# Kernel tuning notes

Hardware: AMD Instinct MI355X
Metric: run time of the kernel (lower is better)

## Reference

```python
import math
import jax, jax.numpy as jnp
import numpy as np

B, T, D = 2048, 50, 256
NEG = -100000.0

def setup_inputs() -> dict:
    key = jax.random.key(0)
    ks = jax.random.split(key, 9)
    return {
        "x": jax.random.normal(ks[0], (B, T, D), dtype=jnp.float32),
        "mask": jax.random.randint(ks[1], (B, T, 1), 0, 2, dtype=jnp.int32),
        "time_decay": jax.random.uniform(ks[2], (B, T, 1), dtype=jnp.float32),
        "Wq": jax.random.normal(ks[3], (D, D), dtype=jnp.float32) * (1.0 / math.sqrt(D)),
        "bq": jax.random.normal(ks[4], (D,), dtype=jnp.float32) * 0.01,
        "Wk": jax.random.normal(ks[5], (D, D), dtype=jnp.float32) * (1.0 / math.sqrt(D)),
        "bk": jax.random.normal(ks[6], (D,), dtype=jnp.float32) * 0.01,
        "Wv": jax.random.normal(ks[7], (D, D), dtype=jnp.float32) * (1.0 / math.sqrt(D)),
        "bv": jax.random.normal(ks[8], (D,), dtype=jnp.float32) * 0.01,
    }

def reference(x, mask, time_decay, Wq, bq, Wk, bk, Wv, bv):
    # PositionalEncoding.forward: elementwise multiply by time-decay (broadcast over d_model)
    x = x * time_decay  # [B,T,D]
    q = jnp.einsum('btd,ed->bte', x, Wq) + bq
    k = jnp.einsum('btd,ed->bte', x, Wk) + bk
    v = jnp.einsum('btd,ed->bte', x, Wv) + bv
    # unusual Q/K-side masking (masked_fill before the matmul)
    keep = mask != 0  # [B,T,1]
    q = jnp.where(keep, q, NEG)
    k = jnp.where(keep, k, NEG)
    score = jnp.einsum('btd,bsd->bts', q, k) / math.sqrt(D)  # [B,T,T]
    score = jax.nn.softmax(score, axis=-1)
    # dropout is identity in eval mode
    out = jnp.einsum('bts,bsd->btd', score, v)  # [B,T,D]
    return out[:, -1, :]  # [B,D]
```

## Files before the change

kernel.cpp:

```cpp
#include <hip/hip_runtime.h>


namespace {
constexpr int kB = 2048;
constexpr int kT = 50;
constexpr int kD = 256;
constexpr int kThr = 256;
constexpr double kNeg = -100000.0;
constexpr int oM2 = 0;
constexpr int oWvp = 65536;
constexpr int oV0 = 131072;
constexpr int oC = 131328;
constexpr int oW1 = 131584;
constexpr int oW2 = 131840;
constexpr int oDbl = 132096;
constexpr int oSq = 132608;
constexpr int oQbk = 136704;
constexpr int oU = 140800;
}

__global__ __launch_bounds__(kThr) void precomp(
    const float* __restrict__ Wq, const float* __restrict__ bq,
    const float* __restrict__ Wk, const float* __restrict__ bk,
    const float* __restrict__ Wv, float* __restrict__ ws) {
  const int t = threadIdx.x;
  const int wave = t >> 6;
  const int lane = t & 63;
  const int blk = blockIdx.x;
  __shared__ float coefL[kD];
  __shared__ double red[3][4];

  if (blk < 256) {
    const int a = blk;
    coefL[t] = Wq[(size_t)t * kD + a];
    __syncthreads();
    const float* kcol = Wk + t;
    float pre[8];
#pragma unroll
    for (int k = 0; k < 8; ++k) pre[k] = kcol[(size_t)k * kD];
    float acc = 0.f;
    for (int j0 = 0; j0 < kD; j0 += 8) {
      float cur[8];
#pragma unroll
      for (int k = 0; k < 8; ++k) cur[k] = pre[k];
      const int nx = (j0 + 8 < kD) ? (j0 + 8) : 0;
#pragma unroll
      for (int k = 0; k < 8; ++k) pre[k] = kcol[(size_t)(nx + k) * kD];
#pragma unroll
      for (int k = 0; k < 8; ++k) acc += coefL[j0 + k] * cur[k];
    }
    ws[oM2 + (a >> 2) * 1024 + 4 * t + (a & 3)] = acc;
  } else if (blk < 258) {
    const float* W = (blk == 256) ? Wk : Wq;
    const float* coef = (blk == 256) ? bq : bk;
    coefL[t] = coef[t];
    __syncthreads();
    const float* col = W + t;
    float pre[8];
#pragma unroll
    for (int k = 0; k < 8; ++k) pre[k] = col[(size_t)k * kD];
    double a0 = 0.0, a1 = 0.0;
    for (int j0 = 0; j0 < kD; j0 += 8) {
      float cur[8];
#pragma unroll
      for (int k = 0; k < 8; ++k) cur[k] = pre[k];
      const int nx = (j0 + 8 < kD) ? (j0 + 8) : 0;
#pragma unroll
      for (int k = 0; k < 8; ++k) pre[k] = col[(size_t)(nx + k) * kD];
#pragma unroll
      for (int k = 0; k < 8; ++k) {
        const double w = (double)cur[k];
        a0 += (double)coefL[j0 + k] * w;
        a1 += w;
      }
    }
    if (blk == 256) {
      ws[oV0 + t] = (float)a0;
      ws[oC + t] = (float)a1;
    } else {
      ws[oW1 + t] = (float)a0;
      ws[oW2 + t] = (float)a1;
      double p0 = (double)bk[t];
      double p1 = (double)bq[t] * (double)bk[t];
      double p2 = (double)bq[t];
#pragma unroll
      for (int off = 32; off; off >>= 1) {
        p0 += __shfl_xor(p0, off);
        p1 += __shfl_xor(p1, off);
        p2 += __shfl_xor(p2, off);
      }
      if (lane == 0) {
        red[0][wave] = p0;
        red[1][wave] = p1;
        red[2][wave] = p2;
      }
      __syncthreads();
      if (t == 0) {
        double* dc = (double*)(ws + oDbl);
        dc[0] = red[0][0] + red[0][1] + red[0][2] + red[0][3];
        dc[1] = red[1][0] + red[1][1] + red[1][2] + red[1][3];
        dc[2] = red[2][0] + red[2][1] + red[2][2] + red[2][3];
      }
    }
  } else {
    const int d4b = (blk - 258) * 4;
    float4 in[4];
#pragma unroll
    for (int k = 0; k < 4; ++k)
      in[k] = *(const float4*)(Wv + (size_t)t * kD + 4 * (d4b + k));
    float4* Wvp = (float4*)(ws + oWvp);
#pragma unroll
    for (int k = 0; k < 4; ++k) Wvp[(size_t)(d4b + k) * kD + t] = in[k];
  }
}

__global__ __launch_bounds__(kThr) void u_gemm(const float* __restrict__ x,
                                               const float* __restrict__ td,
                                               float* __restrict__ ws) {
  const int t = threadIdx.x;
  const int wave = t >> 6;
  const int lane = t & 63;
  const int b0 = blockIdx.x * 4;
  const double* dc = (const double*)(ws + oDbl);

  {
    const int b = b0 + wave;
    const float4 xv =
        ((const float4*)(x + ((size_t)b * kT + kT - 1) * kD))[lane];
    const float4 a1 = ((const float4*)(ws + oW1))[lane];
    const float4 a2 = ((const float4*)(ws + oW2))[lane];
    double s1 = (double)xv.x * a1.x + (double)xv.y * a1.y +
                (double)xv.z * a1.z + (double)xv.w * a1.w;
    double s2 = (double)xv.x * a2.x + (double)xv.y * a2.y +
                (double)xv.z * a2.z + (double)xv.w * a2.w;
#pragma unroll
    for (int off = 32; off; off >>= 1) {
      s1 += __shfl_xor(s1, off);
      s2 += __shfl_xor(s2, off);
    }
    if (lane == 0) {
      const double tdd = (double)td[(size_t)b * kT + kT - 1];
      ((double*)(ws + oQbk))[b] = tdd * s1 + dc[1];
      ((double*)(ws + oSq))[b] = tdd * s2 + dc[2];
    }
  }

  const float4* M2v = (const float4*)(ws + oM2);
  const float4* r0 = (const float4*)(x + ((size_t)(b0 + 0) * kT + kT - 1) * kD);
  const float4* r1 = (const float4*)(x + ((size_t)(b0 + 1) * kT + kT - 1) * kD);
  const float4* r2 = (const float4*)(x + ((size_t)(b0 + 2) * kT + kT - 1) * kD);
  const float4* r3 = (const float4*)(x + ((size_t)(b0 + 3) * kT + kT - 1) * kD);
  const float td0 = td[(size_t)(b0 + 0) * kT + kT - 1];
  const float td1 = td[(size_t)(b0 + 1) * kT + kT - 1];
  const float td2 = td[(size_t)(b0 + 2) * kT + kT - 1];
  const float td3 = td[(size_t)(b0 + 3) * kT + kT - 1];

  float4 pre[8];
#pragma unroll
  for (int k = 0; k < 8; ++k) pre[k] = M2v[(size_t)k * kD + t];
  float acc0 = 0.f, acc1 = 0.f, acc2 = 0.f, acc3 = 0.f;
  for (int j0 = 0; j0 < 64; j0 += 8) {
    float4 cur[8];
#pragma unroll
    for (int k = 0; k < 8; ++k) cur[k] = pre[k];
    const int nx = (j0 + 8 < 64) ? (j0 + 8) : 0;
#pragma unroll
    for (int k = 0; k < 8; ++k) pre[k] = M2v[(size_t)(nx + k) * kD + t];
#pragma unroll
    for (int k = 0; k < 8; ++k) {
      const float4 m = cur[k];
      const float4 x0 = r0[j0 + k];
      const float4 x1 = r1[j0 + k];
      const float4 x2 = r2[j0 + k];
      const float4 x3 = r3[j0 + k];
      acc0 += x0.x * m.x + x0.y * m.y + x0.z * m.z + x0.w * m.w;
      acc1 += x1.x * m.x + x1.y * m.y + x1.z * m.z + x1.w * m.w;
      acc2 += x2.x * m.x + x2.y * m.y + x2.z * m.z + x2.w * m.w;
      acc3 += x3.x * m.x + x3.y * m.y + x3.z * m.z + x3.w * m.w;
    }
  }
  const float v0t = ws[oV0 + t];
  ws[oU + (size_t)(b0 + 0) * kD + t] = td0 * acc0 + v0t;
  ws[oU + (size_t)(b0 + 1) * kD + t] = td1 * acc1 + v0t;
  ws[oU + (size_t)(b0 + 2) * kD + t] = td2 * acc2 + v0t;
  ws[oU + (size_t)(b0 + 3) * kD + t] = td3 * acc3 + v0t;
}

__global__ __launch_bounds__(kThr) void attn(const float* __restrict__ x,
                                             const int* __restrict__ mask,
                                             const float* __restrict__ td,
                                             float* __restrict__ ws) {
  const int t = threadIdx.x;
  const int wave = t >> 6;
  const int lane = t & 63;
  const int b = blockIdx.x * 4 + wave;

  const float mtd = (lane < kT) ? td[(size_t)b * kT + lane] : 0.f;
  const int mmk = (lane < kT) ? mask[(size_t)b * kT + lane] : 0;
  const int mqg = __shfl(mmk, kT - 1);

  const float4 u4 = ((const float4*)(ws + oU))[(size_t)b * 64 + lane];
  const float4 c4 = ((const float4*)(ws + oC))[lane];
  const float4 v4 = mqg ? u4 : c4;

  const double* dcp = (const double*)(ws + oDbl);
  const double sbkd = dcp[0];
  const double Sq = ((const double*)(ws + oSq))[b];
  const double Qbk = ((const double*)(ws + oQbk))[b];
  const double Cm = kNeg * Sq * 0.0625;
  const double Cbb = 256.0 * 1.0e10 * 0.0625;

  const float4* xrow = (const float4*)(x + (size_t)b * kT * kD);
  double m = -1.0e300;
  float l = 0.f;
  float4 y = {0.f, 0.f, 0.f, 0.f};

  float4 n0 = xrow[0 * 64 + lane];
  float4 n1 = xrow[1 * 64 + lane];
  float4 n2 = xrow[2 * 64 + lane];
  float4 n3 = xrow[3 * 64 + lane];
  for (int s = 0; s < 52; s += 4) {
    const float4 r0 = n0, r1 = n1, r2 = n2, r3 = n3;
    {
      const int p0 = (s + 4 < kT) ? s + 4 : kT - 1;
      const int p1 = (s + 5 < kT) ? s + 5 : kT - 1;
      const int p2 = (s + 6 < kT) ? s + 6 : kT - 1;
      const int p3 = (s + 7 < kT) ? s + 7 : kT - 1;
      n0 = xrow[p0 * 64 + lane];
      n1 = xrow[p1 * 64 + lane];
      n2 = xrow[p2 * 64 + lane];
      n3 = xrow[p3 * 64 + lane];
    }
    const int s1i = s + 1, s2i = s + 2, s3i = s + 3;
    const int c0 = s;
    const int c1 = (s1i < kT) ? s1i : kT - 1;
    const int c2 = (s2i < kT) ? s2i : kT - 1;
    const int c3 = (s3i < kT) ? s3i : kT - 1;
    const float tv0 = __shfl(mtd, c0);
    const float tv1 = __shfl(mtd, c1);
    const float tv2 = __shfl(mtd, c2);
    const float tv3 = __shfl(mtd, c3);
    float4 a0, a1, a2, a3;
    a0.x = r0.x * tv0; a0.y = r0.y * tv0; a0.z = r0.z * tv0; a0.w = r0.w * tv0;
    a1.x = r1.x * tv1; a1.y = r1.y * tv1; a1.z = r1.z * tv1; a1.w = r1.w * tv1;
    a2.x = r2.x * tv2; a2.y = r2.y * tv2; a2.z = r2.z * tv2; a2.w = r2.w * tv2;
    a3.x = r3.x * tv3; a3.y = r3.y * tv3; a3.z = r3.z * tv3; a3.w = r3.w * tv3;
    float p0 = a0.x * v4.x + a0.y * v4.y + a0.z * v4.z + a0.w * v4.w;
    float p1 = a1.x * v4.x + a1.y * v4.y + a1.z * v4.z + a1.w * v4.w;
    float p2 = a2.x * v4.x + a2.y * v4.y + a2.z * v4.z + a2.w * v4.w;
    float p3 = a3.x * v4.x + a3.y * v4.y + a3.z * v4.z + a3.w * v4.w;
#pragma unroll
    for (int off = 32; off; off >>= 1) {
      p0 += __shfl_xor(p0, off);
      p1 += __shfl_xor(p1, off);
      p2 += __shfl_xor(p2, off);
      p3 += __shfl_xor(p3, off);
    }
    const int ms0 = __shfl(mmk, c0);
    const int ms1 = __shfl(mmk, c1);
    const int ms2 = __shfl(mmk, c2);
    const int ms3 = __shfl(mmk, c3);
    double sc0, sc1, sc2, sc3;
    if (mqg) {
      sc0 = ms0 ? ((double)p0 + Qbk) * 0.0625 : Cm;
      sc1 = ms1 ? ((double)p1 + Qbk) * 0.0625 : Cm;
      sc2 = ms2 ? ((double)p2 + Qbk) * 0.0625 : Cm;
      sc3 = ms3 ? ((double)p3 + Qbk) * 0.0625 : Cm;
    } else {
      sc0 = ms0 ? kNeg * ((double)p0 + sbkd) * 0.0625 : Cbb;
      sc1 = ms1 ? kNeg * ((double)p1 + sbkd) * 0.0625 : Cbb;
      sc2 = ms2 ? kNeg * ((double)p2 + sbkd) * 0.0625 : Cbb;
      sc3 = ms3 ? kNeg * ((double)p3 + sbkd) * 0.0625 : Cbb;
    }
    if (s1i >= kT) sc1 = -1.0e300;
    if (s2i >= kT) sc2 = -1.0e300;
    if (s3i >= kT) sc3 = -1.0e300;
    double mnew = m;
    if (sc0 > mnew) mnew = sc0;
    if (sc1 > mnew) mnew = sc1;
    if (sc2 > mnew) mnew = sc2;
    if (sc3 > mnew) mnew = sc3;
    const float al = expf((float)(m - mnew));
    const float e0 = expf((float)(sc0 - mnew));
    const float e1 = expf((float)(sc1 - mnew));
    const float e2 = expf((float)(sc2 - mnew));
    const float e3 = expf((float)(sc3 - mnew));
    m = mnew;
    l = l * al + e0 + e1 + e2 + e3;
    y.x = y.x * al + e0 * a0.x + e1 * a1.x + e2 * a2.x + e3 * a3.x;
    y.y = y.y * al + e0 * a0.y + e1 * a1.y + e2 * a2.y + e3 * a3.y;
    y.z = y.z * al + e0 * a0.z + e1 * a1.z + e2 * a2.z + e3 * a3.z;
    y.w = y.w * al + e0 * a0.w + e1 * a1.w + e2 * a2.w + e3 * a3.w;
  }
  const float inv = 1.0f / l;
  y.x *= inv; y.y *= inv; y.z *= inv; y.w *= inv;
  ((float4*)(ws + oU))[(size_t)b * 64 + lane] = y;
}

__global__ __launch_bounds__(kThr) void o_gemm(const float* __restrict__ bv,
                                               const float* __restrict__ ws,
                                               float* __restrict__ out) {
  const int t = threadIdx.x;
  const int b0 = blockIdx.x * 4;
  const float4* Wvv = (const float4*)(ws + oWvp);
  const float4* y0 = (const float4*)(ws + oU + (size_t)(b0 + 0) * kD);
  const float4* y1 = (const float4*)(ws + oU + (size_t)(b0 + 1) * kD);
  const float4* y2 = (const float4*)(ws + oU + (size_t)(b0 + 2) * kD);
  const float4* y3 = (const float4*)(ws + oU + (size_t)(b0 + 3) * kD);

  float4 pre[8];
#pragma unroll
  for (int k = 0; k < 8; ++k) pre[k] = Wvv[(size_t)k * kD + t];
  float acc0 = 0.f, acc1 = 0.f, acc2 = 0.f, acc3 = 0.f;
  for (int j0 = 0; j0 < 64; j0 += 8) {
    float4 cur[8];
#pragma unroll
    for (int k = 0; k < 8; ++k) cur[k] = pre[k];
    const int nx = (j0 + 8 < 64) ? (j0 + 8) : 0;
#pragma unroll
    for (int k = 0; k < 8; ++k) pre[k] = Wvv[(size_t)(nx + k) * kD + t];
#pragma unroll
    for (int k = 0; k < 8; ++k) {
      const float4 m = cur[k];
      const float4 a0 = y0[j0 + k];
      const float4 a1 = y1[j0 + k];
      const float4 a2 = y2[j0 + k];
      const float4 a3 = y3[j0 + k];
      acc0 += a0.x * m.x + a0.y * m.y + a0.z * m.z + a0.w * m.w;
      acc1 += a1.x * m.x + a1.y * m.y + a1.z * m.z + a1.w * m.w;
      acc2 += a2.x * m.x + a2.y * m.y + a2.z * m.z + a2.w * m.w;
      acc3 += a3.x * m.x + a3.y * m.y + a3.z * m.z + a3.w * m.w;
    }
  }
  const float bvt = bv[t];
  out[(size_t)(b0 + 0) * kD + t] = acc0 + bvt;
  out[(size_t)(b0 + 1) * kD + t] = acc1 + bvt;
  out[(size_t)(b0 + 2) * kD + t] = acc2 + bvt;
  out[(size_t)(b0 + 3) * kD + t] = acc3 + bvt;
}

extern "C" void kernel_launch(void* const* d_in, const int* in_sizes, int n_in,
                              void* d_out, int out_size, void* d_ws,
                              size_t ws_size, hipStream_t stream) {
  const float* x = (const float*)d_in[0];
  const int* mask = (const int*)d_in[1];
  const float* td = (const float*)d_in[2];
  const float* Wq = (const float*)d_in[3];
  const float* bq = (const float*)d_in[4];
  const float* Wk = (const float*)d_in[5];
  const float* bk = (const float*)d_in[6];
  const float* Wv = (const float*)d_in[7];
  const float* bv = (const float*)d_in[8];
  float* ws = (float*)d_ws;
  float* out = (float*)d_out;
  (void)in_sizes; (void)n_in; (void)out_size; (void)ws_size;

  hipLaunchKernelGGL(precomp, dim3(274), dim3(kThr), 0, stream, Wq, bq, Wk, bk,
                     Wv, ws);
  hipLaunchKernelGGL(u_gemm, dim3(kB / 4), dim3(kThr), 0, stream, x, td, ws);
  hipLaunchKernelGGL(attn, dim3(kB / 4), dim3(kThr), 0, stream, x, mask, td,
                     ws);
  hipLaunchKernelGGL(o_gemm, dim3(kB / 4), dim3(kThr), 0, stream, bv, ws, out);
}
```

Before: 233.7 us.

## Restructure attention kernel into two-pass softmax with transposed shuffle reduction

The attention kernel now runs one wavefront per block and one batch row per wave. It computes all 50 per-position dot products first and reduces them with a paired butterfly scheme, so each shuffle stage reduces two positions at once. A plain two-pass softmax replaces the online rescaling, with time decay folded into the dot product and the weights. Pass two re-reads x and accumulates the weighted sum. This drops the per-step max/rescale dependency chain and cuts shuffle count, at the cost of reading x twice and higher register use from the unrolled arrays.

```diff
diff --git a/kernel.cpp b/kernel.cpp
--- a/kernel.cpp
+++ b/kernel.cpp
@@ -96,10 +96,10 @@
       }
       __syncthreads();
       if (t == 0) {
-        double* dc = (double*)(ws + oDbl);
-        dc[0] = red[0][0] + red[0][1] + red[0][2] + red[0][3];
-        dc[1] = red[1][0] + red[1][1] + red[1][2] + red[1][3];
-        dc[2] = red[2][0] + red[2][1] + red[2][2] + red[2][3];
+        double* dcw = (double*)(ws + oDbl);
+        dcw[0] = red[0][0] + red[0][1] + red[0][2] + red[0][3];
+        dcw[1] = red[1][0] + red[1][1] + red[1][2] + red[1][3];
+        dcw[2] = red[2][0] + red[2][1] + red[2][2] + red[2][3];
       }
     }
   } else {
@@ -186,18 +186,17 @@
   ws[oU + (size_t)(b0 + 3) * kD + t] = td3 * acc3 + v0t;
 }
 
-__global__ __launch_bounds__(kThr) void attn(const float* __restrict__ x,
-                                             const int* __restrict__ mask,
-                                             const float* __restrict__ td,
-                                             float* __restrict__ ws) {
-  const int t = threadIdx.x;
-  const int wave = t >> 6;
-  const int lane = t & 63;
-  const int b = blockIdx.x * 4 + wave;
-
-  const float mtd = (lane < kT) ? td[(size_t)b * kT + lane] : 0.f;
-  const int mmk = (lane < kT) ? mask[(size_t)b * kT + lane] : 0;
-  const int mqg = __shfl(mmk, kT - 1);
+__global__ __launch_bounds__(64, 2) void attn(const float* __restrict__ x,
+                                              const int* __restrict__ mask,
+                                              const float* __restrict__ td,
+                                              float* __restrict__ ws) {
+  const int lane = threadIdx.x;
+  const int b = blockIdx.x;
+  const int par = lane & 1;
+
+  const int ml = (lane < kT) ? mask[(size_t)b * kT + lane] : 0;
+  const unsigned long long mm = __ballot(ml != 0);
+  const int mqg = (int)((mm >> (kT - 1)) & 1ull);
 
   const float4 u4 = ((const float4*)(ws + oU))[(size_t)b * 64 + lane];
   const float4 c4 = ((const float4*)(ws + oC))[lane];
@@ -211,89 +210,92 @@
   const double Cbb = 256.0 * 1.0e10 * 0.0625;
 
   const float4* xrow = (const float4*)(x + (size_t)b * kT * kD);
-  double m = -1.0e300;
-  float l = 0.f;
+  const float* tdr = td + (size_t)b * kT;
+
+  float dot[kT];
+  {
+    float4 PF[8];
+#pragma unroll
+    for (int i = 0; i < 8; ++i) PF[i] = xrow[i * 64 + lane];
+#pragma unroll
+    for (int s = 0; s < kT; ++s) {
+      const float4 r = PF[s & 7];
+      if (s + 8 < kT) PF[s & 7] = xrow[(s + 8) * 64 + lane];
+      dot[s] = r.x * v4.x + r.y * v4.y + r.z * v4.z + r.w * v4.w;
+    }
+  }
+
+  float R[kT / 2];
+#pragma unroll
+  for (int i = 0; i < kT / 2; ++i) {
+    const float sA = dot[2 * i], sB = dot[2 * i + 1];
+    const float snd = par ? sA : sB;
+    const float o = __shfl_xor(snd, 1);
+    float r = (par ? sB : sA) + o;
+    r += __shfl_xor(r, 2);
+    r += __shfl_xor(r, 4);
+    r += __shfl_xor(r, 8);
+    r += __shfl_xor(r, 16);
+    r += __shfl_xor(r, 32);
+    R[i] = r;
+  }
+
+  double sc[kT / 2];
+#pragma unroll
+  for (int i = 0; i < kT / 2; ++i) {
+    const float tdA = tdr[2 * i], tdB = tdr[2 * i + 1];
+    const double tds = (double)(par ? tdB : tdA);
+    const int msA = (int)((mm >> (2 * i)) & 1ull);
+    const int msB = (int)((mm >> (2 * i + 1)) & 1ull);
+    const int ms = par ? msB : msA;
+    const double xd = tds * (double)R[i];
+    if (mqg)
+      sc[i] = ms ? (xd + Qbk) * 0.0625 : Cm;
+    else
+      sc[i] = ms ? kNeg * (xd + sbkd) * 0.0625 : Cbb;
+  }
+
+  double mloc = sc[0];
+#pragma unroll
+  for (int i = 1; i < kT / 2; ++i) mloc = sc[i] > mloc ? sc[i] : mloc;
+  const double mo = __shfl_xor(mloc, 1);
+  const double m = mloc > mo ? mloc : mo;
+
+  float ef[kT / 2];
+  float lloc = 0.f;
+#pragma unroll
+  for (int i = 0; i < kT / 2; ++i) {
+    ef[i] = expf((float)(sc[i] - m));
+    lloc += ef[i];
+  }
+  const float l = lloc + __shfl_xor(lloc, 1);
+  const float inv = 1.0f / l;
+
+  float wA[kT / 2], wB[kT / 2];
+#pragma unroll
+  for (int i = 0; i < kT / 2; ++i) {
+    const float tdA = tdr[2 * i], tdB = tdr[2 * i + 1];
+    const float wp = ef[i] * inv * (par ? tdB : tdA);
+    wA[i] = __shfl(wp, 0);
+    wB[i] = __shfl(wp, 1);
+  }
+
   float4 y = {0.f, 0.f, 0.f, 0.f};
-
-  float4 n0 = xrow[0 * 64 + lane];
-  float4 n1 = xrow[1 * 64 + lane];
-  float4 n2 = xrow[2 * 64 + lane];
-  float4 n3 = xrow[3 * 64 + lane];
-  for (int s = 0; s < 52; s += 4) {
-    const float4 r0 = n0, r1 = n1, r2 = n2, r3 = n3;
-    {
-      const int p0 = (s + 4 < kT) ? s + 4 : kT - 1;
-      const int p1 = (s + 5 < kT) ? s + 5 : kT - 1;
-      const int p2 = (s + 6 < kT) ? s + 6 : kT - 1;
-      const int p3 = (s + 7 < kT) ? s + 7 : kT - 1;
-      n0 = xrow[p0 * 64 + lane];
-      n1 = xrow[p1 * 64 + lane];
-      n2 = xrow[p2 * 64 + lane];
-      n3 = xrow[p3 * 64 + lane];
-    }
-    const int s1i = s + 1, s2i = s + 2, s3i = s + 3;
-    const int c0 = s;
-    const int c1 = (s1i < kT) ? s1i : kT - 1;
-    const int c2 = (s2i < kT) ? s2i : kT - 1;
-    const int c3 = (s3i < kT) ? s3i : kT - 1;
-    const float tv0 = __shfl(mtd, c0);
-    const float tv1 = __shfl(mtd, c1);
-    const float tv2 = __shfl(mtd, c2);
-    const float tv3 = __shfl(mtd, c3);
-    float4 a0, a1, a2, a3;
-    a0.x = r0.x * tv0; a0.y = r0.y * tv0; a0.z = r0.z * tv0; a0.w = r0.w * tv0;
-    a1.x = r1.x * tv1; a1.y = r1.y * tv1; a1.z = r1.z * tv1; a1.w = r1.w * tv1;
-    a2.x = r2.x * tv2; a2.y = r2.y * tv2; a2.z = r2.z * tv2; a2.w = r2.w * tv2;
-    a3.x = r3.x * tv3; a3.y = r3.y * tv3; a3.z = r3.z * tv3; a3.w = r3.w * tv3;
-    float p0 = a0.x * v4.x + a0.y * v4.y + a0.z * v4.z + a0.w * v4.w;
-    float p1 = a1.x * v4.x + a1.y * v4.y + a1.z * v4.z + a1.w * v4.w;
-    float p2 = a2.x * v4.x + a2.y * v4.y + a2.z * v4.z + a2.w * v4.w;
-    float p3 = a3.x * v4.x + a3.y * v4.y + a3.z * v4.z + a3.w * v4.w;
-#pragma unroll
-    for (int off = 32; off; off >>= 1) {
-      p0 += __shfl_xor(p0, off);
-      p1 += __shfl_xor(p1, off);
-      p2 += __shfl_xor(p2, off);
-      p3 += __shfl_xor(p3, off);
-    }
-    const int ms0 = __shfl(mmk, c0);
-    const int ms1 = __shfl(mmk, c1);
-    const int ms2 = __shfl(mmk, c2);
-    const int ms3 = __shfl(mmk, c3);
-    double sc0, sc1, sc2, sc3;
-    if (mqg) {
-      sc0 = ms0 ? ((double)p0 + Qbk) * 0.0625 : Cm;
-      sc1 = ms1 ? ((double)p1 + Qbk) * 0.0625 : Cm;
-      sc2 = ms2 ? ((double)p2 + Qbk) * 0.0625 : Cm;
-      sc3 = ms3 ? ((double)p3 + Qbk) * 0.0625 : Cm;
-    } else {
-      sc0 = ms0 ? kNeg * ((double)p0 + sbkd) * 0.0625 : Cbb;
-      sc1 = ms1 ? kNeg * ((double)p1 + sbkd) * 0.0625 : Cbb;
-      sc2 = ms2 ? kNeg * ((double)p2 + sbkd) * 0.0625 : Cbb;
-      sc3 = ms3 ? kNeg * ((double)p3 + sbkd) * 0.0625 : Cbb;
-    }
-    if (s1i >= kT) sc1 = -1.0e300;
-    if (s2i >= kT) sc2 = -1.0e300;
-    if (s3i >= kT) sc3 = -1.0e300;
-    double mnew = m;
-    if (sc0 > mnew) mnew = sc0;
-    if (sc1 > mnew) mnew = sc1;
-    if (sc2 > mnew) mnew = sc2;
-    if (sc3 > mnew) mnew = sc3;
-    const float al = expf((float)(m - mnew));
-    const float e0 = expf((float)(sc0 - mnew));
-    const float e1 = expf((float)(sc1 - mnew));
-    const float e2 = expf((float)(sc2 - mnew));
-    const float e3 = expf((float)(sc3 - mnew));
-    m = mnew;
-    l = l * al + e0 + e1 + e2 + e3;
-    y.x = y.x * al + e0 * a0.x + e1 * a1.x + e2 * a2.x + e3 * a3.x;
-    y.y = y.y * al + e0 * a0.y + e1 * a1.y + e2 * a2.y + e3 * a3.y;
-    y.z = y.z * al + e0 * a0.z + e1 * a1.z + e2 * a2.z + e3 * a3.z;
-    y.w = y.w * al + e0 * a0.w + e1 * a1.w + e2 * a2.w + e3 * a3.w;
-  }
-  const float inv = 1.0f / l;
-  y.x *= inv; y.y *= inv; y.z *= inv; y.w *= inv;
+  {
+    float4 PF[8];
+#pragma unroll
+    for (int i = 0; i < 8; ++i) PF[i] = xrow[i * 64 + lane];
+#pragma unroll
+    for (int s = 0; s < kT; ++s) {
+      const float4 r = PF[s & 7];
+      if (s + 8 < kT) PF[s & 7] = xrow[(s + 8) * 64 + lane];
+      const float w = (s & 1) ? wB[s >> 1] : wA[s >> 1];
+      y.x += w * r.x;
+      y.y += w * r.y;
+      y.z += w * r.z;
+      y.w += w * r.w;
+    }
+  }
   ((float4*)(ws + oU))[(size_t)b * 64 + lane] = y;
 }
 
@@ -358,7 +360,6 @@
   hipLaunchKernelGGL(precomp, dim3(274), dim3(kThr), 0, stream, Wq, bq, Wk, bk,
                      Wv, ws);
   hipLaunchKernelGGL(u_gemm, dim3(kB / 4), dim3(kThr), 0, stream, x, td, ws);
-  hipLaunchKernelGGL(attn, dim3(kB / 4), dim3(kThr), 0, stream, x, mask, td,
-                     ws);
+  hipLaunchKernelGGL(attn, dim3(kB), dim3(64), 0, stream, x, mask, td, ws);
   hipLaunchKernelGGL(o_gemm, dim3(kB / 4), dim3(kThr), 0, stream, bv, ws, out);
 }
```

Measured after the change: 245.3 us. +5.0%, slower.
